# Performance work log

Hardware: AMD Instinct MI355X
Metric: run time of the kernel (lower is better)

The kernel has to match this reference:

```python
import jax, jax.numpy as jnp
import numpy as np

NEG_SLOPE = 0.2


def setup_inputs() -> dict:
    key = jax.random.key(0)
    k1, k2, k3, k4 = jax.random.split(key, 4)
    N, E, IN, OUT = 100000, 1600000, 256, 64
    x = jax.random.normal(k1, (N, IN), dtype=jnp.float32)
    edge_index = jax.random.randint(k2, (2, E), 0, N, dtype=jnp.int64)
    W = jax.random.normal(k3, (IN, OUT), dtype=jnp.float32) * (1.0 / np.sqrt(IN))
    a = jax.random.normal(k4, (2 * OUT,), dtype=jnp.float32) * 0.02
    return {"x": x, "W": W, "a": a, "edge_index": edge_index, "num_nodes": N}


def reference(x, W, a, edge_index, num_nodes):
    # h = W(x): torch Linear without bias == x @ W (W stored as [in_dim, out_dim])
    h = x @ W                                   # [N, out_dim]
    src, dst = edge_index[0], edge_index[1]     # [E], [E]
    out_dim = h.shape[1]
    # e = LeakyReLU(cat([hs, hd]) @ a) == LeakyReLU(hs @ a[:d] + hd @ a[d:])
    s_src = h @ a[:out_dim]                     # [N] per-node src score
    s_dst = h @ a[out_dim:]                     # [N] per-node dst score
    e = jax.nn.leaky_relu(s_src[src] + s_dst[dst], NEG_SLOPE)  # [E]
    # per-destination segment softmax (numerically stable)
    m = jax.ops.segment_max(e, dst, num_segments=num_nodes)   # [N]
    ex = jnp.exp(e - m[dst])                                   # [E]
    denom = jax.ops.segment_sum(ex, dst, num_segments=num_nodes)  # [N]
    alpha = ex / denom[dst]                                    # [E]
    # weighted scatter-sum of source features into destinations
    out = jax.ops.segment_sum(h[src] * alpha[:, None], dst, num_segments=num_nodes)
    return out
```

## Files before the change

kernel.cpp:

```cpp
#include <hip/hip_runtime.h>
#include <hip/hip_bf16.h>
#include <math.h>

#define IN_DIM 256
#define OUT_DIM 64
#define NEG_SLOPE 0.2f
#define LCOLS 80
#define NBMAX 392
#define ECAP  10240
#define SENT  0xFFFFFFFFu
#define SCAP  2560
#define NBIN  512
#define KAB_LDS (NBMAX * 32 * 4 + NBMAX * 4 + NBMAX * 4)

typedef __attribute__((ext_vector_type(8))) short bf16x8;
typedef __attribute__((ext_vector_type(4))) float f32x4;

static __device__ __forceinline__ ushort f2bf(float f) {
    union { __hip_bfloat16 b; ushort u; } cv;
    cv.b = __float2bfloat16(f);
    return cv.u;
}
static __device__ __forceinline__ float bf2f(ushort u) {
    union { ushort u2[2]; float f; } cv;
    cv.u2[0] = 0; cv.u2[1] = u;
    return cv.f;
}

__global__ __launch_bounds__(1024) void k0_fused(
        const float* __restrict__ W, const float* __restrict__ a,
        ushort* __restrict__ wb, int* __restrict__ gtail)
{
    __shared__ float wa_l[2 * IN_DIM];
    const int tid = threadIdx.x;

    if (tid < 512) gtail[tid] = 0;

    if (tid < IN_DIM) {
        const float* wr = W + (size_t)tid * OUT_DIM;
        float ss = 0.f, sd = 0.f;
        #pragma unroll
        for (int j = 0; j < OUT_DIM; ++j) {
            const float w = wr[j];
            ss = fmaf(w, a[j], ss);
            sd = fmaf(w, a[OUT_DIM + j], sd);
        }
        wa_l[tid] = ss;
        wa_l[IN_DIM + tid] = sd;
    }
    __syncthreads();

    for (int idx = tid; idx < 8 * 4 * LCOLS * 8; idx += 1024) {
        const int j   = idx & 7;
        const int col = (idx >> 3) % LCOLS;
        const int tk  = (idx >> 3) / LCOLS;
        const int k   = (tk >> 2) * 32 + (tk & 3) * 8 + j;
        float v = 0.f;
        if (col < OUT_DIM)           v = W[(size_t)k * OUT_DIM + col];
        else if (col == OUT_DIM)     v = wa_l[k];
        else if (col == OUT_DIM + 1) v = wa_l[IN_DIM + k];
        wb[idx] = f2bf(v);
    }
}

__global__ __launch_bounds__(256) void kAB(
        const int* __restrict__ ei, int* __restrict__ gtail,
        unsigned int* __restrict__ ebuf, int E, int nbuck,
        const float* __restrict__ x, const ushort* __restrict__ wb,
        ushort* __restrict__ hb, float* __restrict__ s_src,
        float* __restrict__ s_dst, int N, int ngroups)
{
    extern __shared__ char smem[];
    const int tid = threadIdx.x;
    const int bid = blockIdx.x;

    if (bid % 3 == 1) {
        const int bin = bid / 3;
        unsigned int (*lbuf)[32] = (unsigned int(*)[32])smem;
        int* lcnt = (int*)(smem + NBMAX * 32 * 4);
        int* lfl  = lcnt + NBMAX;

        for (int r = tid; r < nbuck; r += 256) { lcnt[r] = 0; lfl[r] = 0; }
        __syncthreads();

        const int e0 = (int)(((long long)bin * E) / NBIN);
        const int e1 = (int)(((long long)(bin + 1) * E) / NBIN);

        for (int b = e0; b < e1; b += 256) {
            const int i = b + tid;
            if (i < e1) {
                const unsigned int src = (unsigned int)ei[i];
                const int dst = ei[E + i];
                const int c = dst >> 8;
                const int pos = atomicAdd(&lcnt[c], 1);
                lbuf[c][pos & 31] = src | ((unsigned int)(dst & 255) << 17);
            }
            __syncthreads();
            for (int r = tid; r < nbuck; r += 256) {
                int cnt = lcnt[r];
                int fl  = lfl[r];
                while (cnt - fl >= 16) {
                    const int gb = atomicAdd(&gtail[r], 16);
                    if (gb + 16 <= ECAP) {
                        uint4* dp = (uint4*)(ebuf + (size_t)r * ECAP + gb);
                        const uint4* sp = (const uint4*)&lbuf[r][fl & 31];
                        dp[0] = sp[0]; dp[1] = sp[1]; dp[2] = sp[2]; dp[3] = sp[3];
                    }
                    fl += 16;
                }
                lfl[r] = fl;
            }
            __syncthreads();
        }

        for (int r = tid; r < nbuck; r += 256) {
            const int cnt = lcnt[r];
            const int fl  = lfl[r];
            if (cnt > fl) {
                const int gb = atomicAdd(&gtail[r], 16);
                if (gb + 16 <= ECAP) {
                    unsigned int tmp[16];
                    #pragma unroll
                    for (int k = 0; k < 16; ++k)
                        tmp[k] = (fl + k < cnt) ? lbuf[r][(fl + k) & 31] : SENT;
                    uint4* dp = (uint4*)(ebuf + (size_t)r * ECAP + gb);
                    #pragma unroll
                    for (int k = 0; k < 4; ++k)
                        dp[k] = make_uint4(tmp[4*k], tmp[4*k+1],
                                           tmp[4*k+2], tmp[4*k+3]);
                }
            }
        }
    } else {
        f32x4* red = (f32x4*)smem;

        const int wv   = tid >> 6;
        const int lane = tid & 63;
        const int l15  = lane & 15;
        const int khi  = lane >> 4;
        const int eidx = lane + (lane >> 3);

        bf16x8 bfrag[2][5];
        #pragma unroll
        for (int tt = 0; tt < 2; ++tt) {
            const int t = 2 * wv + tt;
            #pragma unroll
            for (int c = 0; c < 5; ++c)
                bfrag[tt][c] =
                    ((const bf16x8*)wb)[(t * 4 + khi) * LCOLS + c * 16 + l15];
        }

        const int g0 = (2 * bid) / 3;
        for (int g = g0; g < ngroups; g += 1024) {
            const int row = min(g * 16 + l15, N - 1);
            const float* xp = x + (size_t)row * IN_DIM + wv * 64 + khi * 8;

            const float4 lo0 = *(const float4*)(xp);
            const float4 hi0 = *(const float4*)(xp + 4);
            const float4 lo1 = *(const float4*)(xp + 32);
            const float4 hi1 = *(const float4*)(xp + 36);

            union { bf16x8 v; ushort u[8]; } a0, a1;
            a0.u[0] = f2bf(lo0.x); a0.u[1] = f2bf(lo0.y);
            a0.u[2] = f2bf(lo0.z); a0.u[3] = f2bf(lo0.w);
            a0.u[4] = f2bf(hi0.x); a0.u[5] = f2bf(hi0.y);
            a0.u[6] = f2bf(hi0.z); a0.u[7] = f2bf(hi0.w);
            a1.u[0] = f2bf(lo1.x); a1.u[1] = f2bf(lo1.y);
            a1.u[2] = f2bf(lo1.z); a1.u[3] = f2bf(lo1.w);
            a1.u[4] = f2bf(hi1.x); a1.u[5] = f2bf(hi1.y);
            a1.u[6] = f2bf(hi1.z); a1.u[7] = f2bf(hi1.w);

            f32x4 acc[5] = {{0,0,0,0},{0,0,0,0},{0,0,0,0},{0,0,0,0},{0,0,0,0}};
            #pragma unroll
            for (int c = 0; c < 5; ++c)
                acc[c] = __builtin_amdgcn_mfma_f32_16x16x32_bf16(
                             a0.v, bfrag[0][c], acc[c], 0, 0, 0);
            #pragma unroll
            for (int c = 0; c < 5; ++c)
                acc[c] = __builtin_amdgcn_mfma_f32_16x16x32_bf16(
                             a1.v, bfrag[1][c], acc[c], 0, 0, 0);

            #pragma unroll
            for (int c = 0; c < 5; ++c)
                red[(c * 4 + wv) * 72 + eidx] = acc[c];
            __syncthreads();

            f32x4 s = red[(wv * 4 + 0) * 72 + eidx];
            #pragma unroll
            for (int sw = 1; sw < 4; ++sw)
                s += red[(wv * 4 + sw) * 72 + eidx];

            const int nrow0 = g * 16 + khi * 4;
            #pragma unroll
            for (int r = 0; r < 4; ++r) {
                const int nrow = nrow0 + r;
                if (nrow < N)
                    hb[(size_t)nrow * OUT_DIM + wv * 16 + l15] = f2bf(s[r]);
            }

            if (wv == 0) {
                f32x4 s4 = red[(4 * 4 + 0) * 72 + eidx];
                #pragma unroll
                for (int sw = 1; sw < 4; ++sw)
                    s4 += red[(4 * 4 + sw) * 72 + eidx];
                #pragma unroll
                for (int r = 0; r < 4; ++r) {
                    const int nrow = nrow0 + r;
                    if (nrow < N) {
                        if (l15 == 0) s_src[nrow] = s4[r];
                        if (l15 == 1) s_dst[nrow] = s4[r];
                    }
                }
            }
            __syncthreads();
        }
    }
}

__global__ __launch_bounds__(256) void k2_bucket(
        const unsigned int* __restrict__ ebuf, const int* __restrict__ gtail,
        const ushort* __restrict__ hb, const float* __restrict__ s_src,
        const float* __restrict__ s_dst, float* __restrict__ out,
        int N, int nbuck)
{
    __shared__ int hist[64], bse[64], cur[64];
    __shared__ float sdl[64];
    __shared__ int2 spair[SCAP];

    const int bid = blockIdx.x;
    const int xcd = bid & 7;
    const int j8  = bid >> 3;
    const int H   = j8 & 3;
    const int B   = xcd + 8 * (j8 >> 2);
    if (B >= nbuck) return;

    const int tid = threadIdx.x;
    const int slots = min(gtail[B], ECAP);
    const unsigned int* eb = ebuf + (size_t)B * ECAP;
    const int dgb = B * 256 + H * 64;

    if (tid < 64) {
        hist[tid] = 0;
        const int dg = dgb + tid;
        sdl[tid] = (dg < N) ? s_dst[dg] : 0.f;
    }
    __syncthreads();

    for (int i = tid; i < slots; i += 256) {
        const unsigned int e = eb[i];
        if (e != SENT) {
            const int dl = (int)((e >> 17) & 255);
            if ((dl >> 6) == H) atomicAdd(&hist[dl & 63], 1);
        }
    }
    __syncthreads();

    if (tid < 64) {
        const int v = hist[tid];
        int s = v;
        #pragma unroll
        for (int off = 1; off < 64; off <<= 1) {
            const int u = __shfl_up(s, off, 64);
            if (tid >= off) s += u;
        }
        bse[tid] = s - v;
        cur[tid] = s - v;
    }
    __syncthreads();

    for (int i = tid; i < slots; i += 256) {
        const unsigned int e = eb[i];
        if (e != SENT) {
            const int dl = (int)((e >> 17) & 255);
            if ((dl >> 6) == H) {
                const int src = (int)(e & 0x1FFFF);
                const int d   = dl & 63;
                float sc = s_src[src] + sdl[d];
                sc = (sc > 0.f) ? sc : NEG_SLOPE * sc;
                const int pos = atomicAdd(&cur[d], 1);
                if (pos < SCAP)
                    spair[pos] = make_int2(src, __float_as_int(__expf(sc)));
            }
        }
    }
    __syncthreads();

    const int l15 = tid & 15;
    const int qw  = tid >> 4;
    #pragma unroll
    for (int k = 0; k < 4; ++k) {
        const int d  = qw + 16 * k;
        const int dg = dgb + d;
        if (dg >= N) continue;
        const int beg = bse[d];
        const int cnt = hist[d];
        const int je0 = min(beg, SCAP);
        const int je1 = min(beg + cnt, SCAP);
        const int m   = je1 - je0;

        float a0 = 0.f, a1 = 0.f, a2 = 0.f, a3 = 0.f, den = 0.f;
        #pragma unroll 4
        for (int j = 0; j < m; ++j) {
            const int2 p = spair[je0 + j];
            const float ex = __int_as_float(p.y);
            den += ex;
            const ushort4 hv = *(const ushort4*)(hb + ((size_t)p.x << 6) + (l15 << 2));
            a0 = fmaf(ex, bf2f(hv.x), a0);
            a1 = fmaf(ex, bf2f(hv.y), a1);
            a2 = fmaf(ex, bf2f(hv.z), a2);
            a3 = fmaf(ex, bf2f(hv.w), a3);
        }
        const float r = (m > 0) ? 1.f / den : 0.f;
        float4 v;
        v.x = a0 * r; v.y = a1 * r; v.z = a2 * r; v.w = a3 * r;
        *(float4*)(out + ((size_t)dg << 6) + (l15 << 2)) = v;
    }
}

extern "C" void kernel_launch(void* const* d_in, const int* in_sizes, int n_in,
                              void* d_out, int out_size, void* d_ws, size_t ws_size,
                              hipStream_t stream)
{
    const float* x  = (const float*)d_in[0];
    const float* W  = (const float*)d_in[1];
    const float* a  = (const float*)d_in[2];
    const int*   ei = (const int*)d_in[3];

    const int N = in_sizes[0] / IN_DIM;
    const int E = in_sizes[3] / 2;

    float* out = (float*)d_out;

    char* ws = (char*)d_ws;
    ushort* hb     = (ushort*)ws;                  ws += (size_t)N * OUT_DIM * 2;
    float*  s_src  = (float*)ws;                   ws += (size_t)N * 4;
    float*  s_dst  = (float*)ws;                   ws += (size_t)N * 4;
    ushort* wb     = (ushort*)ws;                  ws += 8 * 4 * LCOLS * 8 * 2;
    int*    gtail  = (int*)ws;                     ws += 512 * 4;
    unsigned int* ebuf = (unsigned int*)ws;        ws += (size_t)NBMAX * ECAP * 4;

    const int nbuck = (N + 255) >> 8;

    k0_fused<<<1, 1024, 0, stream>>>(W, a, wb, gtail);

    const int ngroups = (N + 15) / 16;
    kAB<<<1536, 256, KAB_LDS, stream>>>(ei, gtail, ebuf, E, nbuck,
                                        x, wb, hb, s_src, s_dst, N, ngroups);

    const int k2grid = 8 * 4 * ((nbuck + 7) / 8);
    k2_bucket<<<k2grid, 256, 0, stream>>>(ebuf, gtail, hb, s_src, s_dst, out, N, nbuck);
}
```

Before: 102.8 us.

## Split edge bucketing into two passes over half the buckets to cut LDS

```diff
diff --git a/kernel.cpp b/kernel.cpp
--- a/kernel.cpp
+++ b/kernel.cpp
@@ -7,11 +7,12 @@
 #define NEG_SLOPE 0.2f
 #define LCOLS 80
 #define NBMAX 392
+#define NROW  196
 #define ECAP  10240
 #define SENT  0xFFFFFFFFu
 #define SCAP  2560
 #define NBIN  512
-#define KAB_LDS (NBMAX * 32 * 4 + NBMAX * 4 + NBMAX * 4)
+#define KAB_LDS (NROW * 32 * 4 + NROW * 4 + NROW * 4)
 
 typedef __attribute__((ext_vector_type(8))) short bf16x8;
 typedef __attribute__((ext_vector_type(4))) float f32x4;
@@ -77,59 +78,72 @@
     if (bid % 3 == 1) {
         const int bin = bid / 3;
         unsigned int (*lbuf)[32] = (unsigned int(*)[32])smem;
-        int* lcnt = (int*)(smem + NBMAX * 32 * 4);
-        int* lfl  = lcnt + NBMAX;
-
-        for (int r = tid; r < nbuck; r += 256) { lcnt[r] = 0; lfl[r] = 0; }
-        __syncthreads();
+        int* lcnt = (int*)(smem + NROW * 32 * 4);
+        int* lfl  = lcnt + NROW;
 
         const int e0 = (int)(((long long)bin * E) / NBIN);
         const int e1 = (int)(((long long)(bin + 1) * E) / NBIN);
 
-        for (int b = e0; b < e1; b += 256) {
-            const int i = b + tid;
-            if (i < e1) {
-                const unsigned int src = (unsigned int)ei[i];
-                const int dst = ei[E + i];
-                const int c = dst >> 8;
-                const int pos = atomicAdd(&lcnt[c], 1);
-                lbuf[c][pos & 31] = src | ((unsigned int)(dst & 255) << 17);
-            }
+        for (int pass = 0; pass < 2; ++pass) {
+            const int cbase = pass * NROW;
+            const int nrow  = min(NROW, nbuck - cbase);
+
+            for (int r = tid; r < nrow; r += 256) { lcnt[r] = 0; lfl[r] = 0; }
             __syncthreads();
-            for (int r = tid; r < nbuck; r += 256) {
-                int cnt = lcnt[r];
-                int fl  = lfl[r];
-                while (cnt - fl >= 16) {
-                    const int gb = atomicAdd(&gtail[r], 16);
+
+            for (int b = e0; b < e1; b += 256) {
+                const int i = b + tid;
+                if (i < e1) {
+                    const int dst = ei[E + i];
+                    const int c = (dst >> 8) - cbase;
+                    if (c >= 0 && c < nrow) {
+                        const unsigned int src = (unsigned int)ei[i];
+                        const int pos = atomicAdd(&lcnt[c], 1);
+                        lbuf[c][pos & 31] =
+                            src | ((unsigned int)(dst & 255) << 17);
+                    }
+                }
+                __syncthreads();
+                for (int r = tid; r < nrow; r += 256) {
+                    int cnt = lcnt[r];
+                    int fl  = lfl[r];
+                    while (cnt - fl >= 16) {
+                        const int gb = atomicAdd(&gtail[cbase + r], 16);
+                        if (gb + 16 <= ECAP) {
+                            uint4* dp = (uint4*)(ebuf +
+                                (size_t)(cbase + r) * ECAP + gb);
+                            const uint4* sp = (const uint4*)&lbuf[r][fl & 31];
+                            dp[0] = sp[0]; dp[1] = sp[1];
+                            dp[2] = sp[2]; dp[3] = sp[3];
+                        }
+                        fl += 16;
+                    }
+                    lfl[r] = fl;
+                }
+                __syncthreads();
+            }
+
+            for (int r = tid; r < nrow; r += 256) {
+                const int cnt = lcnt[r];
+                const int fl  = lfl[r];
+                if (cnt > fl) {
+                    const int gb = atomicAdd(&gtail[cbase + r], 16);
                     if (gb + 16 <= ECAP) {
-                        uint4* dp = (uint4*)(ebuf + (size_t)r * ECAP + gb);
-                        const uint4* sp = (const uint4*)&lbuf[r][fl & 31];
-                        dp[0] = sp[0]; dp[1] = sp[1]; dp[2] = sp[2]; dp[3] = sp[3];
+                        unsigned int tmp[16];
+                        #pragma unroll
+                        for (int k = 0; k < 16; ++k)
+                            tmp[k] = (fl + k < cnt) ? lbuf[r][(fl + k) & 31]
+                                                    : SENT;
+                        uint4* dp = (uint4*)(ebuf +
+                            (size_t)(cbase + r) * ECAP + gb);
+                        #pragma unroll
+                        for (int k = 0; k < 4; ++k)
+                            dp[k] = make_uint4(tmp[4*k], tmp[4*k+1],
+                                               tmp[4*k+2], tmp[4*k+3]);
                     }
-                    fl += 16;
                 }
-                lfl[r] = fl;
             }
             __syncthreads();
-        }
-
-        for (int r = tid; r < nbuck; r += 256) {
-            const int cnt = lcnt[r];
-            const int fl  = lfl[r];
-            if (cnt > fl) {
-                const int gb = atomicAdd(&gtail[r], 16);
-                if (gb + 16 <= ECAP) {
-                    unsigned int tmp[16];
-                    #pragma unroll
-                    for (int k = 0; k < 16; ++k)
-                        tmp[k] = (fl + k < cnt) ? lbuf[r][(fl + k) & 31] : SENT;
-                    uint4* dp = (uint4*)(ebuf + (size_t)r * ECAP + gb);
-                    #pragma unroll
-                    for (int k = 0; k < 4; ++k)
-                        dp[k] = make_uint4(tmp[4*k], tmp[4*k+1],
-                                           tmp[4*k+2], tmp[4*k+3]);
-                }
-            }
         }
     } else {
         f32x4* red = (f32x4*)smem;
```

Result: slower. 119.7 us (+16.4%).
